# Performance work log

Measured on AMD Instinct MI355X. Metric: run time of the kernel, lower is better.

The kernel has to match this reference:

```python
import jax, jax.numpy as jnp
import numpy as np

N_HEADS = 4
D_HEAD = 64
SCALE = D_HEAD ** -0.5


def setup_inputs() -> dict:
    key = jax.random.key(0)
    k0, k1, k2, k3, k4 = jax.random.split(key, 5)
    C = 256
    return {
        "x": jax.random.normal(k0, (32, C, 32, 32), dtype=jnp.float32),
        "W_qkv": jax.random.normal(k1, (C, 3 * N_HEADS * D_HEAD), dtype=jnp.float32) * 0.02,
        "b_qkv": jax.random.normal(k2, (3 * N_HEADS * D_HEAD,), dtype=jnp.float32) * 0.02,
        "W_out": jax.random.normal(k3, (C, C), dtype=jnp.float32) * 0.02,
        "b_out": jax.random.normal(k4, (C,), dtype=jnp.float32) * 0.02,
    }


def reference(x, W_qkv, b_qkv, W_out, b_out):
    b, c, h, w = x.shape
    # [B, C, H, W] -> [B, S, C], S = H*W  (NOTE: GroupNorm is defined in the
    # original module but never applied in forward; we match that exactly.)
    xs = x.reshape(b, c, h * w).transpose(0, 2, 1)
    qkv = (xs @ W_qkv + b_qkv).reshape(b, -1, N_HEADS, 3 * D_HEAD)
    q, k, v = jnp.split(qkv, 3, axis=-1)  # each [B, S, H, D]
    scores = jnp.einsum('bihd,bjhd->bijh', q, k) * SCALE  # [B, S, S, H]
    attn = jax.nn.softmax(scores, axis=2)  # softmax over key index j
    res = jnp.einsum('bijh,bjhd->bihd', attn, v).reshape(b, -1, N_HEADS * D_HEAD)
    res = res @ W_out + b_out + xs
    return res.transpose(0, 2, 1).reshape(b, c, h, w)
```

## Files before the change

### kernel.cpp

```cpp
#include <hip/hip_runtime.h>

#define NH 4
#define DH 64
#define SS 1024
#define CC 256
#define BB 32

typedef __attribute__((ext_vector_type(8))) short short8;
typedef __attribute__((ext_vector_type(4))) float floatx4;

#define MFMA16(a, b, c) __builtin_amdgcn_mfma_f32_16x16x32_bf16(a, b, c, 0, 0, 0)

#define QSCALE 0.18033688011112042f

__device__ __forceinline__ short f2bf(float f) {
    union { float f; unsigned u; } v; v.f = f;
    unsigned r = (v.u + 0x7fffu + ((v.u >> 16) & 1u)) >> 16;
    return (short)r;
}
__device__ __forceinline__ unsigned bfrn(float f) {
    union { float f; unsigned u; } v; v.f = f;
    return (v.u + 0x7fffu + ((v.u >> 16) & 1u)) >> 16;
}
__device__ __forceinline__ unsigned pk2_trunc(float a, float b) {
    union { float f; unsigned u; } ua, ub; ua.f = a; ub.f = b;
    return (ua.u >> 16) | (ub.u & 0xFFFF0000u);
}
__device__ __forceinline__ unsigned pk2_rn(float a, float b) {
    return bfrn(a) | (bfrn(b) << 16);
}

__global__ __launch_bounds__(256) void k_prep(const float* __restrict__ x,
                                              const float* __restrict__ Wqkv,
                                              const float* __restrict__ Wout,
                                              short* __restrict__ xs,
                                              short* __restrict__ Wqkv_t,
                                              short* __restrict__ Wout_t) {
    int bid = blockIdx.x;
    if (bid < 2048) {
        __shared__ float tile[64][65];
        int b = bid >> 6;
        int s0 = ((bid >> 2) & 15) * 64;
        int c0 = (bid & 3) * 64;
        int t = threadIdx.x;
        int tx = t & 63, ty = t >> 6;
        for (int i = 0; i < 16; ++i) {
            int c = ty + i * 4;
            tile[tx][c] = x[((b * CC) + (c0 + c)) * SS + s0 + tx];
        }
        __syncthreads();
        for (int i = 0; i < 8; ++i) {
            int s = (t >> 5) + i * 8;
            int cp = (t & 31) * 2;
            short2 v;
            v.x = f2bf(tile[s][cp]);
            v.y = f2bf(tile[s][cp + 1]);
            *(short2*)(&xs[((b * SS) + (s0 + s)) * CC + c0 + cp]) = v;
        }
    } else {
        int idx = (bid - 2048) * 256 + threadIdx.x;
        if (idx < 768 * 256) {
            int n = idx >> 8, k = idx & 255;
            Wqkv_t[idx] = f2bf(Wqkv[k * 768 + n]);
        } else {
            int j = idx - 768 * 256;
            int c = j >> 8, k = j & 255;
            Wout_t[j] = f2bf(Wout[k * 256 + c]);
        }
    }
}

__global__ __launch_bounds__(256) void k_qkv(const short* __restrict__ xs,
                                             const short* __restrict__ Wt,
                                             const float* __restrict__ bqkv,
                                             short* __restrict__ qtw,
                                             short* __restrict__ kw,
                                             short* __restrict__ vtw) {
    __shared__ short smem[10240];
    short* As = smem;
    short* Bs = smem + 5120;
    int bid = blockIdx.x;
    int idx = bid >> 3;
    int m0 = ((bid & 7) * 32 + idx / 6) * 128;
    int n0 = (idx % 6) * 128;
    int t = threadIdx.x;
    int lane = t & 63, wid = t >> 6;
    int wr = wid >> 1, wc = wid & 1;
    int c16 = lane & 15, qd = lane >> 4;

    floatx4 acc[4][4] = {};
    short8 pa[2], pb[2];

    for (int j = 0; j < 2; ++j) {
        int id = j * 256 + t, row = id >> 2, cc = id & 3;
        pa[j] = *(const short8*)(&xs[(m0 + row) * CC + cc * 8]);
        pb[j] = *(const short8*)(&Wt[(n0 + row) * CC + cc * 8]);
    }
    for (int kt = 0; kt < 8; ++kt) {
        if (kt) __syncthreads();
        for (int j = 0; j < 2; ++j) {
            int id = j * 256 + t, row = id >> 2, cc = id & 3;
            *(short8*)(&As[row * 40 + cc * 8]) = pa[j];
            *(short8*)(&Bs[row * 40 + cc * 8]) = pb[j];
        }
        __syncthreads();
        if (kt < 7) {
            for (int j = 0; j < 2; ++j) {
                int id = j * 256 + t, row = id >> 2, cc = id & 3;
                pa[j] = *(const short8*)(&xs[(m0 + row) * CC + (kt + 1) * 32 + cc * 8]);
                pb[j] = *(const short8*)(&Wt[(n0 + row) * CC + (kt + 1) * 32 + cc * 8]);
            }
        }
        short8 av[4], bv[4];
        for (int i = 0; i < 4; ++i) {
            av[i] = *(const short8*)(&As[(wr * 64 + i * 16 + c16) * 40 + qd * 8]);
            bv[i] = *(const short8*)(&Bs[(wc * 64 + i * 16 + c16) * 40 + qd * 8]);
        }
        for (int mi = 0; mi < 4; ++mi)
            for (int ni = 0; ni < 4; ++ni)
                acc[mi][ni] = MFMA16(av[mi], bv[ni], acc[mi][ni]);
    }

    int b = m0 >> 10, sbase = m0 & 1023;
    int seg = (n0 >> 6) + wc;
    int sel = seg % 3, h = seg / 3;
    int bh = b * NH + h;
    float bias4[4];
    for (int ni = 0; ni < 4; ++ni)
        bias4[ni] = bqkv[n0 + wc * 64 + ni * 16 + c16];

    if (sel != 1) {
        float sc = (sel == 0) ? QSCALE : 1.f;
        short* dst = (sel == 0) ? qtw : vtw;
        for (int ni = 0; ni < 4; ++ni) {
            int d = ni * 16 + c16;
            for (int mi = 0; mi < 4; ++mi) {
                int s = sbase + wr * 64 + mi * 16 + qd * 4;
                uint2 ow;
                ow.x = pk2_rn((acc[mi][ni][0] + bias4[ni]) * sc,
                              (acc[mi][ni][1] + bias4[ni]) * sc);
                ow.y = pk2_rn((acc[mi][ni][2] + bias4[ni]) * sc,
                              (acc[mi][ni][3] + bias4[ni]) * sc);
                *(uint2*)(&dst[(size_t)(bh * DH + d) * SS + s]) = ow;
            }
        }
    }

    int seg0 = n0 >> 6;
    int kseg = (seg0 % 3 == 1) ? seg0 : (((seg0 + 1) % 3 == 1) ? seg0 + 1 : -1);
    if (kseg >= 0) {
        short* Kt = smem;
        __syncthreads();
        if (seg == kseg) {
            for (int mi = 0; mi < 4; ++mi)
                for (int ni = 0; ni < 4; ++ni)
                    for (int r = 0; r < 4; ++r)
                        Kt[(wr * 64 + mi * 16 + qd * 4 + r) * 72 + ni * 16 + c16] =
                            f2bf(acc[mi][ni][r] + bias4[ni]);
        }
        __syncthreads();
        int bhk = b * NH + kseg / 3;
        int srow = t >> 1, dh = (t & 1) * 32;
        short* gdst = &kw[(size_t)(bhk * SS + sbase + srow) * DH + dh];
        const short* lsrc = &Kt[srow * 72 + dh];
        for (int k = 0; k < 4; ++k)
            *(short8*)(gdst + k * 8) = *(const short8*)(lsrc + k * 8);
    }
}

__global__ __launch_bounds__(256, 2) void k_attn(const short* __restrict__ qtw,
                                                 const short* __restrict__ kw,
                                                 const short* __restrict__ vtw,
                                                 short* __restrict__ res) {
    __shared__ __align__(16) short Ks[64 * 72];
    __shared__ __align__(16) short Vts[64 * 72];
    __shared__ __align__(16) short Pt[4 * 16 * 76];
    int bid = blockIdx.x;
    int q0 = (bid >> 7) * 256;
    int bh = bid & 127;
    int t = threadIdx.x;
    int lane = t & 63, w = t >> 6;
    int c16 = lane & 15, qd = lane >> 4;
    const short* qp = qtw + (size_t)bh * DH * SS;
    const short* kp = kw + (size_t)bh * SS * DH;
    const short* vp = vtw + (size_t)bh * DH * SS;

    short8 qfrag[4][2];
    for (int g = 0; g < 4; ++g) {
        int s = q0 + g * 64 + w * 16 + c16;
        for (int ks = 0; ks < 2; ++ks) {
            short8 q;
            for (int j = 0; j < 8; ++j)
                q[j] = qp[(size_t)(ks * 32 + qd * 8 + j) * SS + s];
            qfrag[g][ks] = q;
        }
    }

    float l_i[4] = {};
    floatx4 o_acc[4][4] = {};

    short8 kreg[2], vreg[2];
    for (int j = 0; j < 2; ++j) {
        int id = j * 256 + t, row = id >> 3, cc = id & 7;
        kreg[j] = *(const short8*)(&kp[row * DH + cc * 8]);
        vreg[j] = *(const short8*)(&vp[row * SS + cc * 8]);
    }

    int pbase = w * 16 * 76;
    for (int kt = 0; kt < 16; ++kt) {
        if (kt) __syncthreads();
        for (int j = 0; j < 2; ++j) {
            int id = j * 256 + t, row = id >> 3, cc = id & 7;
            *(short8*)(&Ks[row * 72 + cc * 8]) = kreg[j];
            *(short8*)(&Vts[row * 72 + cc * 8]) = vreg[j];
        }
        __syncthreads();
        if (kt < 15) {
            for (int j = 0; j < 2; ++j) {
                int id = j * 256 + t, row = id >> 3, cc = id & 7;
                kreg[j] = *(const short8*)(&kp[((kt + 1) * 64 + row) * DH + cc * 8]);
                vreg[j] = *(const short8*)(&vp[row * SS + (kt + 1) * 64 + cc * 8]);
            }
        }

        short8 kf[2][4], vf[2][4];
        for (int ks = 0; ks < 2; ++ks)
            for (int ji = 0; ji < 4; ++ji) {
                kf[ks][ji] = *(const short8*)(&Ks[(ji * 16 + c16) * 72 + ks * 32 + qd * 8]);
                vf[ks][ji] = *(const short8*)(&Vts[(ji * 16 + c16) * 72 + ks * 32 + qd * 8]);
            }

        for (int g = 0; g < 4; ++g) {
            floatx4 sacc[4] = {};
            for (int ks = 0; ks < 2; ++ks)
                for (int ji = 0; ji < 4; ++ji)
                    sacc[ji] = MFMA16(kf[ks][ji], qfrag[g][ks], sacc[ji]);

            for (int ji = 0; ji < 4; ++ji) {
                float e0 = __builtin_amdgcn_exp2f(sacc[ji][0]);
                float e1 = __builtin_amdgcn_exp2f(sacc[ji][1]);
                float e2 = __builtin_amdgcn_exp2f(sacc[ji][2]);
                float e3 = __builtin_amdgcn_exp2f(sacc[ji][3]);
                l_i[g] += (e0 + e1) + (e2 + e3);
                uint2 pw;
                pw.x = pk2_trunc(e0, e1);
                pw.y = pk2_trunc(e2, e3);
                *(uint2*)(&Pt[pbase + c16 * 76 + ji * 16 + qd * 4]) = pw;
            }

            for (int ks2 = 0; ks2 < 2; ++ks2) {
                short8 pf = *(const short8*)(&Pt[pbase + c16 * 76 + ks2 * 32 + qd * 8]);
                for (int di = 0; di < 4; ++di)
                    o_acc[g][di] = MFMA16(vf[ks2][di], pf, o_acc[g][di]);
            }
        }
    }

    for (int g = 0; g < 4; ++g) {
        float l = l_i[g];
        l += __shfl_xor(l, 16);
        l += __shfl_xor(l, 32);
        l_i[g] = 1.f / l;
    }

    int b = bh >> 2, h = bh & 3;
    for (int g = 0; g < 4; ++g) {
        int s = q0 + g * 64 + w * 16 + c16;
        long base = (long)(b * SS + s) * CC + h * DH;
        float inv = l_i[g];
        for (int di = 0; di < 4; ++di) {
            uint2 ow;
            ow.x = pk2_rn(o_acc[g][di][0] * inv, o_acc[g][di][1] * inv);
            ow.y = pk2_rn(o_acc[g][di][2] * inv, o_acc[g][di][3] * inv);
            *(uint2*)(&res[base + di * 16 + qd * 4]) = ow;
        }
    }
}

__global__ __launch_bounds__(256) void k_out(const short* __restrict__ res,
                                             const short* __restrict__ Wot,
                                             const float* __restrict__ bout,
                                             const float* __restrict__ x,
                                             float* __restrict__ out) {
    __shared__ short As[128 * 40];
    __shared__ short Bs[128 * 40];
    int b = blockIdx.z;
    int m0 = blockIdx.y * 128;
    int n0 = blockIdx.x * 128;
    int t = threadIdx.x;
    int lane = t & 63, wid = t >> 6;
    int wr = wid >> 1, wc = wid & 1;
    int c16 = lane & 15, qd = lane >> 4;

    floatx4 acc[4][4] = {};
    short8 pa[2], pbv[2];
    for (int j = 0; j < 2; ++j) {
        int id = j * 256 + t, row = id >> 2, cc = id & 3;
        pa[j] = *(const short8*)(&Wot[(m0 + row) * CC + cc * 8]);
        pbv[j] = *(const short8*)(&res[(b * SS + n0 + row) * CC + cc * 8]);
    }

    for (int kt = 0; kt < 8; ++kt) {
        if (kt) __syncthreads();
        for (int j = 0; j < 2; ++j) {
            int id = j * 256 + t, row = id >> 2, cc = id & 3;
            *(short8*)(&As[row * 40 + cc * 8]) = pa[j];
            *(short8*)(&Bs[row * 40 + cc * 8]) = pbv[j];
        }
        __syncthreads();
        if (kt < 7) {
            for (int j = 0; j < 2; ++j) {
                int id = j * 256 + t, row = id >> 2, cc = id & 3;
                pa[j] = *(const short8*)(&Wot[(m0 + row) * CC + (kt + 1) * 32 + cc * 8]);
                pbv[j] = *(const short8*)(&res[(b * SS + n0 + row) * CC + (kt + 1) * 32 + cc * 8]);
            }
        }
        short8 av[4], bv[4];
        for (int i = 0; i < 4; ++i) {
            av[i] = *(const short8*)(&As[(wr * 64 + i * 16 + c16) * 40 + qd * 8]);
            bv[i] = *(const short8*)(&Bs[(wc * 64 + i * 16 + c16) * 40 + qd * 8]);
        }
        for (int mi = 0; mi < 4; ++mi)
            for (int ni = 0; ni < 4; ++ni)
                acc[mi][ni] = MFMA16(av[mi], bv[ni], acc[mi][ni]);
    }

    for (int mi = 0; mi < 4; ++mi) {
        for (int r = 0; r < 4; ++r) {
            int c = m0 + wr * 64 + mi * 16 + qd * 4 + r;
            float bias = bout[c];
            for (int ni = 0; ni < 4; ++ni) {
                int s = n0 + wc * 64 + ni * 16 + c16;
                float v = acc[mi][ni][r] + bias + x[((b * CC) + c) * SS + s];
                out[((b * CC) + c) * SS + s] = v;
            }
        }
    }
}

extern "C" void kernel_launch(void* const* d_in, const int* in_sizes, int n_in,
                              void* d_out, int out_size, void* d_ws, size_t ws_size,
                              hipStream_t stream) {
    const float* x    = (const float*)d_in[0];
    const float* Wqkv = (const float*)d_in[1];
    const float* bqkv = (const float*)d_in[2];
    const float* Wout = (const float*)d_in[3];
    const float* bout = (const float*)d_in[4];
    float* out = (float*)d_out;

    char* ws = (char*)d_ws;
    short* xs_res = (short*)(ws);
    short* qtw    = (short*)(ws + 16777216);
    short* kw     = (short*)(ws + 33554432);
    short* vtw    = (short*)(ws + 50331648);
    short* Wqkv_t = (short*)(ws + 67108864);
    short* Wout_t = (short*)(ws + 67502080);

    k_prep<<<dim3(3072), 256, 0, stream>>>(x, Wqkv, Wout, xs_res, Wqkv_t, Wout_t);
    k_qkv<<<dim3(1536), 256, 0, stream>>>(xs_res, Wqkv_t, bqkv, qtw, kw, vtw);
    k_attn<<<dim3(512), 256, 0, stream>>>(qtw, kw, vtw, xs_res);
    k_out<<<dim3(8, 2, 32), 256, 0, stream>>>(xs_res, Wout_t, bout, x, out);
}
```

Before: 176.0 us.

## Switch attention to 32x32x16 MFMA with register-resident P via permlane32 swap

```diff
diff --git a/kernel.cpp b/kernel.cpp
--- a/kernel.cpp
+++ b/kernel.cpp
@@ -8,8 +8,11 @@
 
 typedef __attribute__((ext_vector_type(8))) short short8;
 typedef __attribute__((ext_vector_type(4))) float floatx4;
+typedef __attribute__((ext_vector_type(16))) float floatx16;
+typedef __attribute__((ext_vector_type(2))) unsigned uint2v;
 
 #define MFMA16(a, b, c) __builtin_amdgcn_mfma_f32_16x16x32_bf16(a, b, c, 0, 0, 0)
+#define MFMA32(a, b, c) __builtin_amdgcn_mfma_f32_32x32x16_bf16(a, b, c, 0, 0, 0)
 
 #define QSCALE 0.18033688011112042f
 
@@ -174,30 +177,29 @@
                                                  short* __restrict__ res) {
     __shared__ __align__(16) short Ks[64 * 72];
     __shared__ __align__(16) short Vts[64 * 72];
-    __shared__ __align__(16) short Pt[4 * 16 * 76];
     int bid = blockIdx.x;
     int q0 = (bid >> 7) * 256;
     int bh = bid & 127;
     int t = threadIdx.x;
     int lane = t & 63, w = t >> 6;
-    int c16 = lane & 15, qd = lane >> 4;
+    int l31 = lane & 31, hi = lane >> 5;
     const short* qp = qtw + (size_t)bh * DH * SS;
     const short* kp = kw + (size_t)bh * SS * DH;
     const short* vp = vtw + (size_t)bh * DH * SS;
 
-    short8 qfrag[4][2];
-    for (int g = 0; g < 4; ++g) {
-        int s = q0 + g * 64 + w * 16 + c16;
-        for (int ks = 0; ks < 2; ++ks) {
+    short8 qfrag[2][4];
+    for (int g = 0; g < 2; ++g) {
+        int s = q0 + w * 64 + g * 32 + l31;
+        for (int kd = 0; kd < 4; ++kd) {
             short8 q;
-            for (int j = 0; j < 8; ++j)
-                q[j] = qp[(size_t)(ks * 32 + qd * 8 + j) * SS + s];
-            qfrag[g][ks] = q;
-        }
-    }
-
-    float l_i[4] = {};
-    floatx4 o_acc[4][4] = {};
+            for (int e = 0; e < 8; ++e)
+                q[e] = qp[(size_t)(kd * 16 + hi * 8 + e) * SS + s];
+            qfrag[g][kd] = q;
+        }
+    }
+
+    float l_i[2] = {};
+    floatx16 o_acc[2][2] = {};
 
     short8 kreg[2], vreg[2];
     for (int j = 0; j < 2; ++j) {
@@ -206,7 +208,6 @@
         vreg[j] = *(const short8*)(&vp[row * SS + cc * 8]);
     }
 
-    int pbase = w * 16 * 76;
     for (int kt = 0; kt < 16; ++kt) {
         if (kt) __syncthreads();
         for (int j = 0; j < 2; ++j) {
@@ -224,55 +225,76 @@
         }
 
         short8 kf[2][4], vf[2][4];
-        for (int ks = 0; ks < 2; ++ks)
-            for (int ji = 0; ji < 4; ++ji) {
-                kf[ks][ji] = *(const short8*)(&Ks[(ji * 16 + c16) * 72 + ks * 32 + qd * 8]);
-                vf[ks][ji] = *(const short8*)(&Vts[(ji * 16 + c16) * 72 + ks * 32 + qd * 8]);
-            }
-
-        for (int g = 0; g < 4; ++g) {
-            floatx4 sacc[4] = {};
-            for (int ks = 0; ks < 2; ++ks)
-                for (int ji = 0; ji < 4; ++ji)
-                    sacc[ji] = MFMA16(kf[ks][ji], qfrag[g][ks], sacc[ji]);
-
-            for (int ji = 0; ji < 4; ++ji) {
-                float e0 = __builtin_amdgcn_exp2f(sacc[ji][0]);
-                float e1 = __builtin_amdgcn_exp2f(sacc[ji][1]);
-                float e2 = __builtin_amdgcn_exp2f(sacc[ji][2]);
-                float e3 = __builtin_amdgcn_exp2f(sacc[ji][3]);
-                l_i[g] += (e0 + e1) + (e2 + e3);
-                uint2 pw;
-                pw.x = pk2_trunc(e0, e1);
-                pw.y = pk2_trunc(e2, e3);
-                *(uint2*)(&Pt[pbase + c16 * 76 + ji * 16 + qd * 4]) = pw;
-            }
-
-            for (int ks2 = 0; ks2 < 2; ++ks2) {
-                short8 pf = *(const short8*)(&Pt[pbase + c16 * 76 + ks2 * 32 + qd * 8]);
-                for (int di = 0; di < 4; ++di)
-                    o_acc[g][di] = MFMA16(vf[ks2][di], pf, o_acc[g][di]);
-            }
-        }
-    }
-
-    for (int g = 0; g < 4; ++g) {
+#pragma unroll
+        for (int jt = 0; jt < 2; ++jt)
+#pragma unroll
+            for (int kd = 0; kd < 4; ++kd)
+                kf[jt][kd] = *(const short8*)(&Ks[(jt * 32 + l31) * 72 + kd * 16 + hi * 8]);
+#pragma unroll
+        for (int dt = 0; dt < 2; ++dt)
+#pragma unroll
+            for (int kj = 0; kj < 4; ++kj)
+                vf[dt][kj] = *(const short8*)(&Vts[(dt * 32 + l31) * 72 + kj * 16 + hi * 8]);
+
+#pragma unroll
+        for (int g = 0; g < 2; ++g) {
+#pragma unroll
+            for (int jt = 0; jt < 2; ++jt) {
+                floatx16 sacc = {};
+                __builtin_amdgcn_s_setprio(1);
+#pragma unroll
+                for (int kd = 0; kd < 4; ++kd)
+                    sacc = MFMA32(kf[jt][kd], qfrag[g][kd], sacc);
+                __builtin_amdgcn_s_setprio(0);
+
+                float ls = 0.f;
+                unsigned u[8];
+#pragma unroll
+                for (int r = 0; r < 16; r += 2) {
+                    float e0 = __builtin_amdgcn_exp2f(sacc[r]);
+                    float e1 = __builtin_amdgcn_exp2f(sacc[r + 1]);
+                    ls += e0 + e1;
+                    u[r >> 1] = pk2_trunc(e0, e1);
+                }
+                l_i[g] += ls;
+
+                uint2v r02 = __builtin_amdgcn_permlane32_swap(u[0], u[2], false, false);
+                uint2v r13 = __builtin_amdgcn_permlane32_swap(u[1], u[3], false, false);
+                uint2v r46 = __builtin_amdgcn_permlane32_swap(u[4], u[6], false, false);
+                uint2v r57 = __builtin_amdgcn_permlane32_swap(u[5], u[7], false, false);
+                union { unsigned w[4]; short8 s; } pf0, pf1;
+                pf0.w[0] = r02[0]; pf0.w[1] = r13[0]; pf0.w[2] = r02[1]; pf0.w[3] = r13[1];
+                pf1.w[0] = r46[0]; pf1.w[1] = r57[0]; pf1.w[2] = r46[1]; pf1.w[3] = r57[1];
+
+                __builtin_amdgcn_s_setprio(1);
+#pragma unroll
+                for (int dt = 0; dt < 2; ++dt) {
+                    o_acc[g][dt] = MFMA32(vf[dt][jt * 2 + 0], pf0.s, o_acc[g][dt]);
+                    o_acc[g][dt] = MFMA32(vf[dt][jt * 2 + 1], pf1.s, o_acc[g][dt]);
+                }
+                __builtin_amdgcn_s_setprio(0);
+            }
+        }
+    }
+
+    int b = bh >> 2, h = bh & 3;
+#pragma unroll
+    for (int g = 0; g < 2; ++g) {
         float l = l_i[g];
-        l += __shfl_xor(l, 16);
         l += __shfl_xor(l, 32);
-        l_i[g] = 1.f / l;
-    }
-
-    int b = bh >> 2, h = bh & 3;
-    for (int g = 0; g < 4; ++g) {
-        int s = q0 + g * 64 + w * 16 + c16;
+        float inv = 1.f / l;
+        int s = q0 + w * 64 + g * 32 + l31;
         long base = (long)(b * SS + s) * CC + h * DH;
-        float inv = l_i[g];
-        for (int di = 0; di < 4; ++di) {
-            uint2 ow;
-            ow.x = pk2_rn(o_acc[g][di][0] * inv, o_acc[g][di][1] * inv);
-            ow.y = pk2_rn(o_acc[g][di][2] * inv, o_acc[g][di][3] * inv);
-            *(uint2*)(&res[base + di * 16 + qd * 4]) = ow;
+#pragma unroll
+        for (int dt = 0; dt < 2; ++dt) {
+#pragma unroll
+            for (int q = 0; q < 4; ++q) {
+                int d = dt * 32 + q * 8 + hi * 4;
+                uint2 ow;
+                ow.x = pk2_rn(o_acc[g][dt][q * 4 + 0] * inv, o_acc[g][dt][q * 4 + 1] * inv);
+                ow.y = pk2_rn(o_acc[g][dt][q * 4 + 2] * inv, o_acc[g][dt][q * 4 + 3] * inv);
+                *(uint2*)(&res[base + d]) = ow;
+            }
         }
     }
 }
```

New measurement: 200.1 us. 1.14x slower.
